# Performance work log

Measured on AMD Instinct MI355X. Metric: run time of the kernel, lower is better.

Reference implementation:

```python
import jax, jax.numpy as jnp
import numpy as np

ROPE_BASE = 10000.0

def _rope(x):
    # x: (B, S, D); canonical interleaved RoPE over sequence positions
    B, S, D = x.shape
    half = D // 2
    inv_freq = 1.0 / (ROPE_BASE ** (jnp.arange(half, dtype=x.dtype) * 2.0 / D))  # (half,)
    ang = jnp.arange(S, dtype=x.dtype)[:, None] * inv_freq[None, :]              # (S, half)
    cos, sin = jnp.cos(ang), jnp.sin(ang)
    x1 = x[..., 0::2]   # (B, S, half)
    x2 = x[..., 1::2]
    rot = jnp.stack([x1 * cos - x2 * sin, x1 * sin + x2 * cos], axis=-1)         # (B,S,half,2)
    return rot.reshape(B, S, D)

def setup_inputs() -> dict:
    key = jax.random.key(0)
    ks = jax.random.split(key, 7)
    B, S, D = 32, 1024, 768
    sc = 1.0 / np.sqrt(D)
    return {
        "x":  jax.random.normal(ks[0], (B, S, D), dtype=jnp.float32),
        "Wq": jax.random.normal(ks[1], (D, D), dtype=jnp.float32) * sc,
        "bq": jax.random.normal(ks[2], (D,), dtype=jnp.float32) * 0.01,
        "Wk": jax.random.normal(ks[3], (D, D), dtype=jnp.float32) * sc,
        "bk": jax.random.normal(ks[4], (D,), dtype=jnp.float32) * 0.01,
        "Wv": jax.random.normal(ks[5], (D, D), dtype=jnp.float32) * sc,
        "bv": jax.random.normal(ks[6], (D,), dtype=jnp.float32) * 0.01,
    }

def reference(x, Wq, bq, Wk, bk, Wv, bv):
    D = x.shape[-1]
    # torch nn.Linear: y = x @ W.T + b
    Q = jnp.einsum('bsd,ed->bse', x, Wq) + bq
    K = jnp.einsum('bsd,ed->bse', x, Wk) + bk
    V = jnp.einsum('bsd,ed->bse', x, Wv) + bv
    Q = _rope(Q)
    K = _rope(K)
    scores = jnp.einsum('bqd,bkd->bqk', Q, K) / jnp.sqrt(jnp.asarray(D, x.dtype))
    weights = jax.nn.softmax(scores, axis=-1)
    return jnp.einsum('bqk,bkd->bqd', weights, V)
```

## Files before the change

### kernel.cpp

```cpp
#include <hip/hip_runtime.h>


typedef __attribute__((ext_vector_type(8))) _Float16 f16x8;
typedef __attribute__((ext_vector_type(4))) float    f32x4;

__device__ __forceinline__ unsigned short f2h(float f) {
    _Float16 h = (_Float16)f;
    return __builtin_bit_cast(unsigned short, h);
}

__device__ __forceinline__ void async_ld16(const void* g, void* l) {
    __builtin_amdgcn_global_load_lds(
        (const __attribute__((address_space(1))) void*)g,
        (__attribute__((address_space(3))) void*)l, 16, 0, 0);
}

template<int MODE, int KDIM, int LDA, int LDB>
__global__ __launch_bounds__(256)
void gemm_bt(const unsigned short* __restrict__ A,
             const unsigned short* __restrict__ B,
             void* __restrict__ C0, void* __restrict__ C1,
             const float* __restrict__ bias0,
             const float* __restrict__ bias1,
             float scale)
{
    __shared__ __align__(16) unsigned short sA[128 * 32];
    __shared__ __align__(16) unsigned short sB[128 * 32];

    const int tid  = threadIdx.x;
    const int lane = tid & 63;
    const int wave = tid >> 6;
    const int wrow = (wave >> 1) * 64;
    const int wcol = (wave & 1) * 64;
    const int quad = lane >> 4;
    const int l15  = lane & 15;

    int m0, n0, z = 0;
    if constexpr (MODE == 0) {
        m0 = (blockIdx.x & 255) * 128;  n0 = (blockIdx.x >> 8) * 128;
    } else if constexpr (MODE == 1) {
        n0 = (blockIdx.x & 255) * 128;  m0 = (blockIdx.x >> 8) * 128;
    } else if constexpr (MODE == 2) {
        z = blockIdx.x & 31; const int q = blockIdx.x >> 5;
        m0 = (q >> 3) * 128; n0 = (q & 7) * 128;
    } else {
        z = blockIdx.x & 31; const int q = blockIdx.x >> 5;
        m0 = (q / 6) * 128;  n0 = (q % 6) * 128;
    }

    const unsigned short* Ab = A;
    const unsigned short* Bb = B;
    if constexpr (MODE == 2) { Ab += (size_t)z * 786432;  Bb += (size_t)z * 786432; }
    if constexpr (MODE == 3) { Ab += (size_t)z * 1048576; Bb += (size_t)z * 786432; }

    const int srow0 = tid >> 2;
    const int sk    = (tid & 3) * 8;

    f32x4 acc[4][4] = {};

    for (int kt = 0; kt < KDIM; kt += 32) {
        __syncthreads();
        async_ld16(Ab + (size_t)(m0 +      srow0) * LDA + kt + sk, &sA[tid * 8]);
        async_ld16(Ab + (size_t)(m0 + 64 + srow0) * LDA + kt + sk, &sA[2048 + tid * 8]);
        async_ld16(Bb + (size_t)(n0 +      srow0) * LDB + kt + sk, &sB[tid * 8]);
        async_ld16(Bb + (size_t)(n0 + 64 + srow0) * LDB + kt + sk, &sB[2048 + tid * 8]);
        __syncthreads();

        f16x8 af[4], bfr[4];
        #pragma unroll
        for (int mi = 0; mi < 4; ++mi)
            af[mi] = *(const f16x8*)&sA[(wrow + mi * 16 + l15) * 32 + quad * 8];
        #pragma unroll
        for (int ni = 0; ni < 4; ++ni)
            bfr[ni] = *(const f16x8*)&sB[(wcol + ni * 16 + l15) * 32 + quad * 8];

        #pragma unroll
        for (int mi = 0; mi < 4; ++mi)
            #pragma unroll
            for (int ni = 0; ni < 4; ++ni)
                acc[mi][ni] = __builtin_amdgcn_mfma_f32_16x16x32_f16(
                    af[mi], bfr[ni], acc[mi][ni], 0, 0, 0);
    }

    #pragma unroll
    for (int mi = 0; mi < 4; ++mi) {
        #pragma unroll
        for (int ni = 0; ni < 4; ++ni) {
            #pragma unroll
            for (int reg = 0; reg < 4; ++reg) {
                const int grow = m0 + wrow + mi * 16 + quad * 4 + reg;
                const int gcol = n0 + wcol + ni * 16 + l15;
                float v = acc[mi][ni][reg];
                if constexpr (MODE == 0) {
                    const bool isQ = gcol < 768;
                    const int  col = isQ ? gcol : gcol - 768;
                    v += isQ ? bias0[col] : bias1[col];
                    const float other = __shfl_xor(v, 1);
                    const int   s     = grow & 1023;
                    const float invf  = exp2f((float)(col >> 1) * -0.03460341765507773f);
                    const float ang   = (float)s * invf;
                    float sn, cs;
                    __sincosf(ang, &sn, &cs);
                    float r = (col & 1) ? (other * sn + v * cs)
                                        : (v * cs - other * sn);
                    if (isQ) r *= scale;
                    unsigned short* dst = (unsigned short*)(isQ ? C0 : C1);
                    dst[(size_t)grow * 768 + col] = f2h(r);
                } else if constexpr (MODE == 1) {
                    v += bias0[grow];
                    const int b = gcol >> 10, s = gcol & 1023;
                    ((unsigned short*)C0)[(size_t)b * (768 * 1024)
                                          + (size_t)grow * 1024 + s] = f2h(v);
                } else if constexpr (MODE == 2) {
                    (((float*)C0) + (size_t)z * 1048576)[(size_t)grow * 1024 + gcol] = v;
                } else {
                    (((float*)C0) + (size_t)z * 786432)[(size_t)grow * 768 + gcol] = v;
                }
            }
        }
    }
}

__global__ __launch_bounds__(256)
void softmax_rows(const float* __restrict__ S, unsigned short* __restrict__ P)
{
    const int row = blockIdx.x;
    const int tid = threadIdx.x;
    const float4 v = ((const float4*)(S + (size_t)row * 1024))[tid];

    float m = fmaxf(fmaxf(v.x, v.y), fmaxf(v.z, v.w));
    #pragma unroll
    for (int o = 1; o < 64; o <<= 1) m = fmaxf(m, __shfl_xor(m, o));
    __shared__ float redm[4];
    __shared__ float reds[4];
    const int wave = tid >> 6, lane = tid & 63;
    if (lane == 0) redm[wave] = m;
    __syncthreads();
    m = fmaxf(fmaxf(redm[0], redm[1]), fmaxf(redm[2], redm[3]));

    const float e0 = __expf(v.x - m), e1 = __expf(v.y - m);
    const float e2 = __expf(v.z - m), e3 = __expf(v.w - m);
    float sum = e0 + e1 + e2 + e3;
    #pragma unroll
    for (int o = 1; o < 64; o <<= 1) sum += __shfl_xor(sum, o);
    if (lane == 0) reds[wave] = sum;
    __syncthreads();
    sum = reds[0] + reds[1] + reds[2] + reds[3];
    const float inv = 1.0f / sum;

    ushort4 o4;
    o4.x = f2h(e0 * inv); o4.y = f2h(e1 * inv);
    o4.z = f2h(e2 * inv); o4.w = f2h(e3 * inv);
    ((ushort4*)(P + (size_t)row * 1024))[tid] = o4;
}

__global__ void cvt_f32_f16(const float4* __restrict__ in,
                            ushort4* __restrict__ out, int n4)
{
    int i = blockIdx.x * 256 + threadIdx.x;
    const int stride = gridDim.x * 256;
    for (; i < n4; i += stride) {
        const float4 v = in[i];
        ushort4 o;
        o.x = f2h(v.x); o.y = f2h(v.y); o.z = f2h(v.z); o.w = f2h(v.w);
        out[i] = o;
    }
}

extern "C" void kernel_launch(void* const* d_in, const int* in_sizes, int n_in,
                              void* d_out, int out_size, void* d_ws, size_t ws_size,
                              hipStream_t stream)
{
    const float* x  = (const float*)d_in[0];
    const float* Wq = (const float*)d_in[1];
    const float* bq = (const float*)d_in[2];
    const float* Wk = (const float*)d_in[3];
    const float* bk = (const float*)d_in[4];
    const float* Wv = (const float*)d_in[5];
    const float* bv = (const float*)d_in[6];
    float* out = (float*)d_out;

    char* ws = (char*)d_ws;
    unsigned short* xh  = (unsigned short*)(ws + 0);
    unsigned short* wqk = (unsigned short*)(ws + 50331648);
    unsigned short* wvh = (unsigned short*)(ws + 52690944);
    unsigned short* Qh  = (unsigned short*)(ws + 53870592);
    unsigned short* Kh  = (unsigned short*)(ws + 104202240);
    unsigned short* Vt  = (unsigned short*)(ws + 154533888);
    float*          Sc  = (float*)         (ws + 204865536);
    unsigned short* Ph  = (unsigned short*)(ws + 0);

    cvt_f32_f16<<<4096, 256, 0, stream>>>((const float4*)x,  (ushort4*)xh, 25165824 / 4);
    cvt_f32_f16<<<576,  256, 0, stream>>>((const float4*)Wq, (ushort4*)wqk, 589824 / 4);
    cvt_f32_f16<<<576,  256, 0, stream>>>((const float4*)Wk, (ushort4*)(wqk + 589824), 589824 / 4);
    cvt_f32_f16<<<576,  256, 0, stream>>>((const float4*)Wv, (ushort4*)wvh, 589824 / 4);

    const float qscale = 0.03608439182435161f;

    gemm_bt<0, 768, 768, 768><<<3072, 256, 0, stream>>>(
        xh, wqk, Qh, Kh, bq, bk, qscale);
    gemm_bt<1, 768, 768, 768><<<1536, 256, 0, stream>>>(
        wvh, xh, Vt, nullptr, bv, nullptr, 1.0f);
    gemm_bt<2, 768, 768, 768><<<2048, 256, 0, stream>>>(
        Qh, Kh, Sc, nullptr, nullptr, nullptr, 1.0f);
    softmax_rows<<<32768, 256, 0, stream>>>(Sc, Ph);
    gemm_bt<3, 1024, 1024, 1024><<<1536, 256, 0, stream>>>(
        Ph, Vt, out, nullptr, nullptr, nullptr, 1.0f);
}
```

Measured before the change: 600.2 us.

## Widen GEMM K tile with swizzled LDS, pack stores, store scores as fp16

The GEMM K step grows from 32 to 64, using XOR-swizzled LDS addressing to avoid bank conflicts and halve the number of barriers. Epilogue stores are packed pairwise through lane shuffles into 32-bit or float2 writes, and the RoPE inverse frequencies are hoisted out of the inner loop. The attention score matrix is written as fp16 instead of fp32, halving its write and its re-read in the softmax. This risks precision loss or overflow in the fp16 scores, though Q is pre-scaled.

```diff
diff --git a/kernel.cpp b/kernel.cpp
--- a/kernel.cpp
+++ b/kernel.cpp
@@ -7,6 +7,9 @@
 __device__ __forceinline__ unsigned short f2h(float f) {
     _Float16 h = (_Float16)f;
     return __builtin_bit_cast(unsigned short, h);
+}
+__device__ __forceinline__ float h2f(unsigned short u) {
+    return (float)__builtin_bit_cast(_Float16, u);
 }
 
 __device__ __forceinline__ void async_ld16(const void* g, void* l) {
@@ -24,8 +27,8 @@
              const float* __restrict__ bias1,
              float scale)
 {
-    __shared__ __align__(16) unsigned short sA[128 * 32];
-    __shared__ __align__(16) unsigned short sB[128 * 32];
+    __shared__ __align__(16) unsigned short sA[128 * 64];
+    __shared__ __align__(16) unsigned short sB[128 * 64];
 
     const int tid  = threadIdx.x;
     const int lane = tid & 63;
@@ -53,33 +56,54 @@
     if constexpr (MODE == 2) { Ab += (size_t)z * 786432;  Bb += (size_t)z * 786432; }
     if constexpr (MODE == 3) { Ab += (size_t)z * 1048576; Bb += (size_t)z * 786432; }
 
-    const int srow0 = tid >> 2;
-    const int sk    = (tid & 3) * 8;
+    const int srow = tid >> 3;
+    const int sk   = ((tid & 7) ^ (srow & 7)) * 8;
 
     f32x4 acc[4][4] = {};
 
-    for (int kt = 0; kt < KDIM; kt += 32) {
+    for (int kt = 0; kt < KDIM; kt += 64) {
         __syncthreads();
-        async_ld16(Ab + (size_t)(m0 +      srow0) * LDA + kt + sk, &sA[tid * 8]);
-        async_ld16(Ab + (size_t)(m0 + 64 + srow0) * LDA + kt + sk, &sA[2048 + tid * 8]);
-        async_ld16(Bb + (size_t)(n0 +      srow0) * LDB + kt + sk, &sB[tid * 8]);
-        async_ld16(Bb + (size_t)(n0 + 64 + srow0) * LDB + kt + sk, &sB[2048 + tid * 8]);
+        #pragma unroll
+        for (int g = 0; g < 4; ++g) {
+            async_ld16(Ab + (size_t)(m0 + g * 32 + srow) * LDA + kt + sk,
+                       &sA[g * 2048 + tid * 8]);
+            async_ld16(Bb + (size_t)(n0 + g * 32 + srow) * LDB + kt + sk,
+                       &sB[g * 2048 + tid * 8]);
+        }
         __syncthreads();
 
-        f16x8 af[4], bfr[4];
-        #pragma unroll
-        for (int mi = 0; mi < 4; ++mi)
-            af[mi] = *(const f16x8*)&sA[(wrow + mi * 16 + l15) * 32 + quad * 8];
-        #pragma unroll
-        for (int ni = 0; ni < 4; ++ni)
-            bfr[ni] = *(const f16x8*)&sB[(wcol + ni * 16 + l15) * 32 + quad * 8];
-
-        #pragma unroll
-        for (int mi = 0; mi < 4; ++mi)
-            #pragma unroll
-            for (int ni = 0; ni < 4; ++ni)
-                acc[mi][ni] = __builtin_amdgcn_mfma_f32_16x16x32_f16(
-                    af[mi], bfr[ni], acc[mi][ni], 0, 0, 0);
+        #pragma unroll
+        for (int kk = 0; kk < 2; ++kk) {
+            f16x8 af[4], bfr[4];
+            #pragma unroll
+            for (int mi = 0; mi < 4; ++mi) {
+                const int r = wrow + mi * 16 + l15;
+                af[mi] = *(const f16x8*)&sA[r * 64 + (((kk * 4 + quad) ^ (r & 7)) << 3)];
+            }
+            #pragma unroll
+            for (int ni = 0; ni < 4; ++ni) {
+                const int r = wcol + ni * 16 + l15;
+                bfr[ni] = *(const f16x8*)&sB[r * 64 + (((kk * 4 + quad) ^ (r & 7)) << 3)];
+            }
+            #pragma unroll
+            for (int mi = 0; mi < 4; ++mi)
+                #pragma unroll
+                for (int ni = 0; ni < 4; ++ni)
+                    acc[mi][ni] = __builtin_amdgcn_mfma_f32_16x16x32_f16(
+                        af[mi], bfr[ni], acc[mi][ni], 0, 0, 0);
+        }
+    }
+
+    const bool evenlane = (l15 & 1) == 0;
+
+    float invf[4];
+    if constexpr (MODE == 0) {
+        #pragma unroll
+        for (int ni = 0; ni < 4; ++ni) {
+            int col = n0 + wcol + ni * 16 + l15;
+            if (col >= 768) col -= 768;
+            invf[ni] = exp2f((float)(col >> 1) * -0.03460341765507773f);
+        }
     }
 
     #pragma unroll
@@ -97,24 +121,44 @@
                     v += isQ ? bias0[col] : bias1[col];
                     const float other = __shfl_xor(v, 1);
                     const int   s     = grow & 1023;
-                    const float invf  = exp2f((float)(col >> 1) * -0.03460341765507773f);
-                    const float ang   = (float)s * invf;
+                    const float ang   = (float)s * invf[ni];
                     float sn, cs;
                     __sincosf(ang, &sn, &cs);
-                    float r = (col & 1) ? (other * sn + v * cs)
-                                        : (v * cs - other * sn);
+                    float r = (col & 1) ? fmaf(other, sn, v * cs)
+                                        : fmaf(v, cs, -(other * sn));
                     if (isQ) r *= scale;
-                    unsigned short* dst = (unsigned short*)(isQ ? C0 : C1);
-                    dst[(size_t)grow * 768 + col] = f2h(r);
+                    const unsigned short h = f2h(r);
+                    const unsigned int packed =
+                        (unsigned int)h | (__shfl_xor((unsigned int)h, 1) << 16);
+                    if (evenlane) {
+                        unsigned short* dst = (unsigned short*)(isQ ? C0 : C1);
+                        *(unsigned int*)(dst + (size_t)grow * 768 + col) = packed;
+                    }
                 } else if constexpr (MODE == 1) {
                     v += bias0[grow];
-                    const int b = gcol >> 10, s = gcol & 1023;
-                    ((unsigned short*)C0)[(size_t)b * (768 * 1024)
-                                          + (size_t)grow * 1024 + s] = f2h(v);
+                    const unsigned short h = f2h(v);
+                    const unsigned int packed =
+                        (unsigned int)h | (__shfl_xor((unsigned int)h, 1) << 16);
+                    if (evenlane) {
+                        const int b = gcol >> 10, s = gcol & 1023;
+                        *(unsigned int*)((unsigned short*)C0 + (size_t)b * (768 * 1024)
+                                         + (size_t)grow * 1024 + s) = packed;
+                    }
                 } else if constexpr (MODE == 2) {
-                    (((float*)C0) + (size_t)z * 1048576)[(size_t)grow * 1024 + gcol] = v;
+                    const unsigned short h = f2h(v);
+                    const unsigned int packed =
+                        (unsigned int)h | (__shfl_xor((unsigned int)h, 1) << 16);
+                    if (evenlane) {
+                        *(unsigned int*)((unsigned short*)C0 + (size_t)z * 1048576
+                                         + (size_t)grow * 1024 + gcol) = packed;
+                    }
                 } else {
-                    (((float*)C0) + (size_t)z * 786432)[(size_t)grow * 768 + gcol] = v;
+                    const float vo = __shfl_xor(v, 1);
+                    if (evenlane) {
+                        float2 p; p.x = v; p.y = vo;
+                        *(float2*)(((float*)C0) + (size_t)z * 786432
+                                   + (size_t)grow * 768 + gcol) = p;
+                    }
                 }
             }
         }
@@ -122,13 +166,14 @@
 }
 
 __global__ __launch_bounds__(256)
-void softmax_rows(const float* __restrict__ S, unsigned short* __restrict__ P)
+void softmax_rows(const unsigned short* __restrict__ S, unsigned short* __restrict__ P)
 {
     const int row = blockIdx.x;
     const int tid = threadIdx.x;
-    const float4 v = ((const float4*)(S + (size_t)row * 1024))[tid];
-
-    float m = fmaxf(fmaxf(v.x, v.y), fmaxf(v.z, v.w));
+    const ushort4 u = ((const ushort4*)(S + (size_t)row * 1024))[tid];
+    const float v0 = h2f(u.x), v1 = h2f(u.y), v2 = h2f(u.z), v3 = h2f(u.w);
+
+    float m = fmaxf(fmaxf(v0, v1), fmaxf(v2, v3));
     #pragma unroll
     for (int o = 1; o < 64; o <<= 1) m = fmaxf(m, __shfl_xor(m, o));
     __shared__ float redm[4];
@@ -138,8 +183,8 @@
     __syncthreads();
     m = fmaxf(fmaxf(redm[0], redm[1]), fmaxf(redm[2], redm[3]));
 
-    const float e0 = __expf(v.x - m), e1 = __expf(v.y - m);
-    const float e2 = __expf(v.z - m), e3 = __expf(v.w - m);
+    const float e0 = __expf(v0 - m), e1 = __expf(v1 - m);
+    const float e2 = __expf(v2 - m), e3 = __expf(v3 - m);
     float sum = e0 + e1 + e2 + e3;
     #pragma unroll
     for (int o = 1; o < 64; o <<= 1) sum += __shfl_xor(sum, o);
@@ -187,7 +232,7 @@
     unsigned short* Qh  = (unsigned short*)(ws + 53870592);
     unsigned short* Kh  = (unsigned short*)(ws + 104202240);
     unsigned short* Vt  = (unsigned short*)(ws + 154533888);
-    float*          Sc  = (float*)         (ws + 204865536);
+    unsigned short* Sc  = (unsigned short*)(ws + 204865536);
     unsigned short* Ph  = (unsigned short*)(ws + 0);
 
     cvt_f32_f16<<<4096, 256, 0, stream>>>((const float4*)x,  (ushort4*)xh, 25165824 / 4);
```

Result: faster. 572.4 us (-4.6%).
